# Performance work log

Hardware: AMD Instinct MI355X
Metric: run time of the kernel (lower is better)

## Reference

```python
import jax, jax.numpy as jnp
import numpy as np
import math

B, N, XD, ED, H = 8, 128, 256, 128, 8
DF = XD // H
FFX, FFE = 1024, 512


def _lin(x, w, b):
    return x @ w + b


def _ln(x, g, b):
    m = x.mean(-1, keepdims=True)
    v = ((x - m) ** 2).mean(-1, keepdims=True)
    return (x - m) / jnp.sqrt(v + 1e-5) * g + b


def setup_inputs() -> dict:
    key = jax.random.key(0)
    ks = jax.random.split(key, 16)
    d = {}
    d['x'] = jax.random.normal(ks[0], (B, N, XD), jnp.float32)
    d['e'] = jax.random.normal(ks[1], (B, N, N, ED), jnp.float32)
    wspecs = [('wq', (XD, XD)), ('wk', (XD, XD)), ('wv', (XD, XD)),
              ('wem', (ED, XD)), ('wea', (ED, XD)), ('wxo', (XD, XD)),
              ('weo', (XD, ED)), ('wx1', (XD, FFX)), ('wx2', (FFX, XD)),
              ('we1', (ED, FFE)), ('we2', (FFE, ED))]
    for i, (name, shp) in enumerate(wspecs):
        d[name] = jax.random.normal(ks[2 + i % 14], shp, jnp.float32) * 0.02
        d[name] = jax.random.normal(jax.random.fold_in(key, i + 10), shp, jnp.float32) * 0.02
    for name, dim in [('bq', XD), ('bk', XD), ('bv', XD), ('bem', XD), ('bea', XD),
                      ('bxo', XD), ('beo', ED), ('bx1', FFX), ('bx2', XD),
                      ('be1', FFE), ('be2', ED)]:
        d[name] = jnp.zeros((dim,), jnp.float32)
    d['gnx'] = jnp.ones((XD,), jnp.float32)
    d['bnx'] = jnp.zeros((XD,), jnp.float32)
    d['gne'] = jnp.ones((ED,), jnp.float32)
    d['bne'] = jnp.zeros((ED,), jnp.float32)
    return d


def reference(x, e, wq, wk, wv, wem, wea, wxo, weo, wx1, wx2, we1, we2,
              bq, bk, bv, bem, bea, bxo, beo, bx1, bx2, be1, be2,
              gnx, bnx, gne, bne):
    # --- NodeEdgeBlock ---
    Q = _lin(x, wq, bq).reshape(B, N, H, DF)
    K = _lin(x, wk, bk).reshape(B, N, H, DF)
    # per-channel outer product: (B, N_i, N_j, H, DF)
    Y = Q[:, :, None] * K[:, None] / math.sqrt(DF)
    E1 = _lin(e, wem, bem).reshape(B, N, N, H, DF)
    E2 = _lin(e, wea, bea).reshape(B, N, N, H, DF)
    Y = Y * (E1 + 1.0) + E2
    newE = _lin(Y.reshape(B, N, N, XD), weo, beo)
    attn = jax.nn.softmax(Y, axis=1)  # softmax over source-node axis i
    V = _lin(x, wv, bv := bv if False else bv).reshape(B, N, H, DF) if False else _lin(x, wv, bv).reshape(B, N, H, DF)
    wV = (attn * V[:, None]).sum(axis=1).reshape(B, N, XD)
    newX = _lin(wV, wxo, bxo)

    # --- FF blocks (dropout=0 => identity); note the SAME norm (norm2) is applied twice,
    # and the second residual uses the pre-norm input, matching the torch code. ---
    def ff(inp, new, w1, b1, w2, b2, g, bn):
        h = _ln(inp + new, g, bn)
        h = jax.nn.relu(_lin(h, w1, b1))
        h = _lin(h, w2, b2)
        return _ln(inp + h, g, bn)

    x_out = ff(x, newX, wx1, bx1, wx2, bx2, gnx, bnx)
    e_out = ff(e, newE, we1, be1, we2, be2, gne, bne)
    return (x_out, e_out)
```

## Files before the change

kernel.cpp:

```cpp
#include <hip/hip_runtime.h>


#define RSQRT_DF 0.17677669529663687f

typedef __attribute__((ext_vector_type(8))) short short8;
typedef __attribute__((ext_vector_type(4))) short short4v;
typedef __attribute__((ext_vector_type(4))) float f32x4;

__device__ __forceinline__ short f2bs(float f) {
    unsigned u = __float_as_uint(f);
    unsigned r = u + 0x7FFFu + ((u >> 16) & 1u);
    return (short)(r >> 16);
}
__device__ __forceinline__ float bs2f(short s) {
    return __uint_as_float(((unsigned)(unsigned short)s) << 16);
}

struct PackArgs {
    const float* W[11];
    short* Wp[11];
    int kdiv[11];
    int N[11];
    int start[12];
};

__global__ __launch_bounds__(256) void pack_all(PackArgs pa) {
    int g = blockIdx.x * 256 + threadIdx.x;
    if (g >= pa.start[11]) return;
    int i = 0;
    while (g >= pa.start[i + 1]) ++i;
    int local = g - pa.start[i];
    int kdiv = pa.kdiv[i], N = pa.N[i];
    int lane = local & 63, rest = local >> 6;
    int kb = rest % kdiv, nt = rest / kdiv;
    int n = nt * 16 + (lane & 15);
    int k0 = kb * 32 + ((lane >> 4) << 3);
    const float* W = pa.W[i];
    short8 v;
#pragma unroll
    for (int j = 0; j < 8; ++j) v[j] = f2bs(W[(size_t)(k0 + j) * N + n]);
    *(short8*)(pa.Wp[i] + (size_t)local * 8) = v;
}

__global__ __launch_bounds__(256) void qk_gemm(
    const float* __restrict__ x,
    const short* __restrict__ wqP, const short* __restrict__ wkP,
    const float* __restrict__ bq, const float* __restrict__ bk,
    float* __restrict__ Qb, float* __restrict__ Kb) {
    __shared__ short sXb[16 * 264];
    const int t = threadIdx.x, wave = t >> 6, lane = t & 63;
    const int quad = lane >> 4, l15 = lane & 15;
    const int m0 = (blockIdx.x & 63) * 16;
    const int isK = blockIdx.x >> 6;
    const short* wP = isK ? wkP : wqP;
    const float* bp = isK ? bk : bq;
    float* outp = isK ? Kb : Qb;

    const float4* x4 = (const float4*)(x + (size_t)m0 * 256);
    for (int g = t; g < 1024; g += 256) {
        float4 v = x4[g];
        int row = g >> 6, col4 = (g & 63) * 4;
        short4v sv = {f2bs(v.x), f2bs(v.y), f2bs(v.z), f2bs(v.w)};
        *(short4v*)(sXb + row * 264 + col4) = sv;
    }
    __syncthreads();

#pragma unroll 2
    for (int p = 0; p < 4; ++p) {
        int nt = wave * 4 + p;
        f32x4 acc = (f32x4){0.f, 0.f, 0.f, 0.f};
        const short* aB = sXb + l15 * 264 + quad * 8;
        const short* bB = wP + ((size_t)(nt * 8) * 64 + lane) * 8;
#pragma unroll
        for (int kb = 0; kb < 8; ++kb) {
            short8 a = *(const short8*)(aB + kb * 32);
            short8 w = *(const short8*)(bB + (size_t)kb * 512);
            acc = __builtin_amdgcn_mfma_f32_16x16x32_bf16(a, w, acc, 0, 0, 0);
        }
        int col = nt * 16 + l15;
        float bvv = bp[col];
#pragma unroll
        for (int r = 0; r < 4; ++r)
            outp[(size_t)(m0 + quad * 4 + r) * 256 + col] = acc[r] + bvv;
    }
}

__global__ __launch_bounds__(256, 3) void fused_main(
    const float* __restrict__ x, const float* __restrict__ e,
    const float* __restrict__ Qb, const float* __restrict__ Kb,
    const short* __restrict__ wvP, const short* __restrict__ wxoP,
    const short* __restrict__ wx1P, const short* __restrict__ wx2P,
    const short* __restrict__ wemP, const short* __restrict__ weaP,
    const short* __restrict__ weoP, const short* __restrict__ we1P,
    const short* __restrict__ we2P,
    const float* __restrict__ bv, const float* __restrict__ bxo,
    const float* __restrict__ bx1, const float* __restrict__ bx2,
    const float* __restrict__ bem, const float* __restrict__ bea,
    const float* __restrict__ beo, const float* __restrict__ be1,
    const float* __restrict__ be2,
    const float* __restrict__ gnx, const float* __restrict__ bnx,
    const float* __restrict__ gne, const float* __restrict__ bne,
    float* __restrict__ xout, float* __restrict__ eout) {
    __shared__ __align__(16) char ldsbuf[51200];
    const int t = threadIdx.x, wave = t >> 6, lane = t & 63;
    const int quad = lane >> 4, l15 = lane & 15;

    if (blockIdx.x < 64) {
        short* sXb = (short*)ldsbuf;
        short* sVb = (short*)(ldsbuf + 8448);
        short* sTbx = (short*)(ldsbuf + 16896);
        float* sRx = (float*)(ldsbuf + 25344);
        short* sH1x = (short*)(ldsbuf + 25344);
        float* sH2x = (float*)(ldsbuf + 25344);
        const int m0 = blockIdx.x * 16;

        const float4* x4 = (const float4*)(x + (size_t)m0 * 256);
        for (int g = t; g < 1024; g += 256) {
            float4 v = x4[g];
            int row = g >> 6, col4 = (g & 63) * 4;
            short4v sv = {f2bs(v.x), f2bs(v.y), f2bs(v.z), f2bs(v.w)};
            *(short4v*)(sXb + row * 264 + col4) = sv;
        }
        __syncthreads();

#pragma unroll 2
        for (int p = 0; p < 4; ++p) {
            int nt = wave * 4 + p;
            f32x4 acc = (f32x4){0.f, 0.f, 0.f, 0.f};
            const short* aB = sXb + l15 * 264 + quad * 8;
            const short* bB = wvP + ((size_t)(nt * 8) * 64 + lane) * 8;
#pragma unroll
            for (int kb = 0; kb < 8; ++kb) {
                short8 a = *(const short8*)(aB + kb * 32);
                short8 w = *(const short8*)(bB + (size_t)kb * 512);
                acc = __builtin_amdgcn_mfma_f32_16x16x32_bf16(a, w, acc, 0, 0, 0);
            }
            int col = nt * 16 + l15;
            float bvv = bv[col];
#pragma unroll
            for (int r = 0; r < 4; ++r)
                sVb[(quad * 4 + r) * 264 + col] = f2bs(acc[r] + bvv);
        }
        __syncthreads();

#pragma unroll 2
        for (int p = 0; p < 4; ++p) {
            int nt = wave * 4 + p;
            f32x4 acc = (f32x4){0.f, 0.f, 0.f, 0.f};
            const short* aB = sVb + l15 * 264 + quad * 8;
            const short* bB = wxoP + ((size_t)(nt * 8) * 64 + lane) * 8;
#pragma unroll
            for (int kb = 0; kb < 8; ++kb) {
                short8 a = *(const short8*)(aB + kb * 32);
                short8 w = *(const short8*)(bB + (size_t)kb * 512);
                acc = __builtin_amdgcn_mfma_f32_16x16x32_bf16(a, w, acc, 0, 0, 0);
            }
            int col = nt * 16 + l15;
            float bvv = bxo[col];
#pragma unroll
            for (int r = 0; r < 4; ++r)
                sRx[(quad * 4 + r) * 260 + col] = acc[r] + bvv;
        }
        __syncthreads();

        for (int rr = 0; rr < 4; ++rr) {
            int row = wave * 4 + rr;
            float v[4];
            float s1 = 0.f, s2 = 0.f;
#pragma unroll
            for (int k = 0; k < 4; ++k) {
                v[k] = bs2f(sXb[row * 264 + lane + 64 * k]) + sRx[row * 260 + lane + 64 * k];
                s1 += v[k]; s2 += v[k] * v[k];
            }
            for (int off = 32; off; off >>= 1) {
                s1 += __shfl_down(s1, off);
                s2 += __shfl_down(s2, off);
            }
            s1 = __shfl(s1, 0); s2 = __shfl(s2, 0);
            float mean = s1 * (1.f / 256.f);
            float var = s2 * (1.f / 256.f) - mean * mean;
            float rstd = rsqrtf(var + 1e-5f);
#pragma unroll
            for (int k = 0; k < 4; ++k)
                sTbx[row * 264 + lane + 64 * k] =
                    f2bs((v[k] - mean) * rstd * gnx[lane + 64 * k] + bnx[lane + 64 * k]);
        }
        __syncthreads();

        f32x4 accE[4];
#pragma unroll
        for (int p = 0; p < 4; ++p) accE[p] = (f32x4){0.f, 0.f, 0.f, 0.f};
        for (int half = 0; half < 2; ++half) {
#pragma unroll 2
            for (int p = 0; p < 8; ++p) {
                int ntg = half * 32 + wave * 8 + p;
                int coll = (wave * 8 + p) * 16 + l15;
                f32x4 acc = (f32x4){0.f, 0.f, 0.f, 0.f};
                const short* aB = sTbx + l15 * 264 + quad * 8;
                const short* bB = wx1P + ((size_t)(ntg * 8) * 64 + lane) * 8;
#pragma unroll
                for (int kb = 0; kb < 8; ++kb) {
                    short8 a = *(const short8*)(aB + kb * 32);
                    short8 w = *(const short8*)(bB + (size_t)kb * 512);
                    acc = __builtin_amdgcn_mfma_f32_16x16x32_bf16(a, w, acc, 0, 0, 0);
                }
                float bvv = bx1[ntg * 16 + l15];
#pragma unroll
                for (int r = 0; r < 4; ++r)
                    sH1x[(quad * 4 + r) * 520 + coll] = f2bs(fmaxf(acc[r] + bvv, 0.f));
            }
            __syncthreads();
#pragma unroll 2
            for (int p = 0; p < 4; ++p) {
                int nt = wave * 4 + p;
                const short* aB = sH1x + l15 * 520 + quad * 8;
                const short* bB = wx2P + ((size_t)(nt * 32 + half * 16) * 64 + lane) * 8;
#pragma unroll
                for (int kb = 0; kb < 16; ++kb) {
                    short8 a = *(const short8*)(aB + kb * 32);
                    short8 w = *(const short8*)(bB + (size_t)kb * 512);
                    accE[p] = __builtin_amdgcn_mfma_f32_16x16x32_bf16(a, w, accE[p], 0, 0, 0);
                }
            }
            __syncthreads();
        }
#pragma unroll
        for (int p = 0; p < 4; ++p) {
            int nt = wave * 4 + p;
            int col = nt * 16 + l15;
            float bvv = bx2[col];
#pragma unroll
            for (int r = 0; r < 4; ++r)
                sH2x[(quad * 4 + r) * 260 + col] = accE[p][r] + bvv;
        }
        __syncthreads();

        for (int rr = 0; rr < 4; ++rr) {
            int row = wave * 4 + rr;
            float v[4];
            float s1 = 0.f, s2 = 0.f;
#pragma unroll
            for (int k = 0; k < 4; ++k) {
                v[k] = bs2f(sXb[row * 264 + lane + 64 * k]) + sH2x[row * 260 + lane + 64 * k];
                s1 += v[k]; s2 += v[k] * v[k];
            }
            for (int off = 32; off; off >>= 1) {
                s1 += __shfl_down(s1, off);
                s2 += __shfl_down(s2, off);
            }
            s1 = __shfl(s1, 0); s2 = __shfl(s2, 0);
            float mean = s1 * (1.f / 256.f);
            float var = s2 * (1.f / 256.f) - mean * mean;
            float rstd = rsqrtf(var + 1e-5f);
#pragma unroll
            for (int k = 0; k < 4; ++k)
                xout[(size_t)(m0 + row) * 256 + lane + 64 * k] =
                    (v[k] - mean) * rstd * gnx[lane + 64 * k] + bnx[lane + 64 * k];
        }
        return;
    }

    short* sEb = (short*)ldsbuf;
    short* sTb = (short*)(ldsbuf + 8704);
    float* sR  = (float*)(ldsbuf + 17408);
    short* sH1 = (short*)(ldsbuf + 17408);
    short* sYb = (short*)(ldsbuf + 34304);
    float* sH2 = (float*)(ldsbuf + 34304);

    const int r0 = (blockIdx.x - 64) * 32;
    const int b = r0 >> 14;
    const int j0 = r0 & 127;

    float g0 = gne[lane], g1 = gne[lane + 64];
    float bn0 = bne[lane], bn1 = bne[lane + 64];

    float qk[2][4][4];
#pragma unroll
    for (int ntl = 0; ntl < 4; ++ntl) {
        const int col = (wave * 4 + ntl) * 16 + l15;
        const float q = Qb[(size_t)(r0 >> 7) * 256 + col] * RSQRT_DF;
#pragma unroll
        for (int mt = 0; mt < 2; ++mt) {
            const float* kp = Kb + (size_t)((b << 7) + j0 + mt * 16 + quad * 4) * 256 + col;
#pragma unroll
            for (int r = 0; r < 4; ++r) qk[mt][ntl][r] = q * kp[(size_t)r * 256];
        }
    }

    {
        const float4* e4 = (const float4*)(e + (size_t)r0 * 128);
        for (int g = t; g < 1024; g += 256) {
            float4 v = e4[g];
            int row = g >> 5, col4 = (g & 31) * 4;
            short4v sv = {f2bs(v.x), f2bs(v.y), f2bs(v.z), f2bs(v.w)};
            *(short4v*)(sEb + row * 136 + col4) = sv;
        }
    }
    __syncthreads();

    {
        short8 aE[2][4];
#pragma unroll
        for (int mt = 0; mt < 2; ++mt)
#pragma unroll
            for (int kb = 0; kb < 4; ++kb)
                aE[mt][kb] = *(const short8*)(sEb + (mt * 16 + l15) * 136 + quad * 8 + kb * 32);
#pragma unroll
        for (int ntl = 0; ntl < 4; ++ntl) {
            const int nt = wave * 4 + ntl;
            const short* b1 = wemP + ((size_t)(nt * 4) * 64 + lane) * 8;
            const short* b2 = weaP + ((size_t)(nt * 4) * 64 + lane) * 8;
            short8 w1[4], w2[4];
#pragma unroll
            for (int kb = 0; kb < 4; ++kb) {
                w1[kb] = *(const short8*)(b1 + (size_t)kb * 512);
                w2[kb] = *(const short8*)(b2 + (size_t)kb * 512);
            }
            const int col = nt * 16 + l15;
            const float bm = bem[col], ba = bea[col];
#pragma unroll
            for (int mt = 0; mt < 2; ++mt) {
                f32x4 a1 = (f32x4){0.f, 0.f, 0.f, 0.f};
                f32x4 a2 = (f32x4){0.f, 0.f, 0.f, 0.f};
#pragma unroll
                for (int kb = 0; kb < 4; ++kb) {
                    a1 = __builtin_amdgcn_mfma_f32_16x16x32_bf16(aE[mt][kb], w1[kb], a1, 0, 0, 0);
                    a2 = __builtin_amdgcn_mfma_f32_16x16x32_bf16(aE[mt][kb], w2[kb], a2, 0, 0, 0);
                }
#pragma unroll
                for (int r = 0; r < 4; ++r) {
                    int row = mt * 16 + quad * 4 + r;
                    float y = qk[mt][ntl][r] * (a1[r] + bm + 1.0f) + (a2[r] + ba);
                    sYb[row * 264 + col] = f2bs(y);
                }
            }
        }
    }
    __syncthreads();

    {
        short8 aY[2][8];
#pragma unroll
        for (int mt = 0; mt < 2; ++mt)
#pragma unroll
            for (int kb = 0; kb < 8; ++kb)
                aY[mt][kb] = *(const short8*)(sYb + (mt * 16 + l15) * 264 + quad * 8 + kb * 32);
#pragma unroll
        for (int ntl = 0; ntl < 2; ++ntl) {
            const int nt = wave * 2 + ntl;
            const short* bB = weoP + ((size_t)(nt * 8) * 64 + lane) * 8;
            short8 w[8];
#pragma unroll
            for (int kb = 0; kb < 8; ++kb) w[kb] = *(const short8*)(bB + (size_t)kb * 512);
            const int col = nt * 16 + l15;
            const float bo = beo[col];
#pragma unroll
            for (int mt = 0; mt < 2; ++mt) {
                f32x4 acc = (f32x4){0.f, 0.f, 0.f, 0.f};
#pragma unroll
                for (int kb = 0; kb < 8; ++kb)
                    acc = __builtin_amdgcn_mfma_f32_16x16x32_bf16(aY[mt][kb], w[kb], acc, 0, 0, 0);
#pragma unroll
                for (int r = 0; r < 4; ++r)
                    sR[(mt * 16 + quad * 4 + r) * 132 + col] = acc[r] + bo;
            }
        }
    }
    __syncthreads();

    for (int rr = 0; rr < 8; ++rr) {
        int row = wave * 8 + rr;
        float v0 = bs2f(sEb[row * 136 + lane]) + sR[row * 132 + lane];
        float v1 = bs2f(sEb[row * 136 + lane + 64]) + sR[row * 132 + lane + 64];
        float s1 = v0 + v1, s2 = v0 * v0 + v1 * v1;
        for (int off = 32; off; off >>= 1) {
            s1 += __shfl_down(s1, off);
            s2 += __shfl_down(s2, off);
        }
        s1 = __shfl(s1, 0); s2 = __shfl(s2, 0);
        float mean = s1 * 0.0078125f;
        float var = s2 * 0.0078125f - mean * mean;
        float rstd = rsqrtf(var + 1e-5f);
        sTb[row * 136 + lane]      = f2bs((v0 - mean) * rstd * g0 + bn0);
        sTb[row * 136 + lane + 64] = f2bs((v1 - mean) * rstd * g1 + bn1);
    }
    __syncthreads();

    f32x4 accE[4];
#pragma unroll
    for (int p = 0; p < 4; ++p) accE[p] = (f32x4){0.f, 0.f, 0.f, 0.f};

    for (int half = 0; half < 2; ++half) {
        short8 aT[2][4];
#pragma unroll
        for (int mt = 0; mt < 2; ++mt)
#pragma unroll
            for (int kb = 0; kb < 4; ++kb)
                aT[mt][kb] = *(const short8*)(sTb + (mt * 16 + l15) * 136 + quad * 8 + kb * 32);
#pragma unroll
        for (int ntl = 0; ntl < 4; ++ntl) {
            const int ntg = half * 16 + wave * 4 + ntl;
            const short* bB = we1P + ((size_t)(ntg * 4) * 64 + lane) * 8;
            short8 w[4];
#pragma unroll
            for (int kb = 0; kb < 4; ++kb) w[kb] = *(const short8*)(bB + (size_t)kb * 512);
            const int coll = (wave * 4 + ntl) * 16 + l15;
            const float bvv = be1[ntg * 16 + l15];
#pragma unroll
            for (int mt = 0; mt < 2; ++mt) {
                f32x4 acc = (f32x4){0.f, 0.f, 0.f, 0.f};
#pragma unroll
                for (int kb = 0; kb < 4; ++kb)
                    acc = __builtin_amdgcn_mfma_f32_16x16x32_bf16(aT[mt][kb], w[kb], acc, 0, 0, 0);
#pragma unroll
                for (int r = 0; r < 4; ++r)
                    sH1[(mt * 16 + quad * 4 + r) * 264 + coll] = f2bs(fmaxf(acc[r] + bvv, 0.f));
            }
        }
        __syncthreads();
        {
            short8 aH[2][8];
#pragma unroll
            for (int mt = 0; mt < 2; ++mt)
#pragma unroll
                for (int kb = 0; kb < 8; ++kb)
                    aH[mt][kb] = *(const short8*)(sH1 + (mt * 16 + l15) * 264 + quad * 8 + kb * 32);
#pragma unroll
            for (int ntl = 0; ntl < 2; ++ntl) {
                const int nt = wave * 2 + ntl;
                const short* bB = we2P + ((size_t)(nt * 16 + half * 8) * 64 + lane) * 8;
                short8 w[8];
#pragma unroll
                for (int kb = 0; kb < 8; ++kb) w[kb] = *(const short8*)(bB + (size_t)kb * 512);
#pragma unroll
                for (int mt = 0; mt < 2; ++mt) {
#pragma unroll
                    for (int kb = 0; kb < 8; ++kb)
                        accE[ntl * 2 + mt] = __builtin_amdgcn_mfma_f32_16x16x32_bf16(
                            aH[mt][kb], w[kb], accE[ntl * 2 + mt], 0, 0, 0);
                }
            }
        }
        __syncthreads();
    }
#pragma unroll
    for (int ntl = 0; ntl < 2; ++ntl)
#pragma unroll
        for (int mt = 0; mt < 2; ++mt) {
            const int nt = wave * 2 + ntl;
            const int col = nt * 16 + l15;
            const float bvv = be2[col];
#pragma unroll
            for (int r = 0; r < 4; ++r)
                sH2[(mt * 16 + quad * 4 + r) * 132 + col] = accE[ntl * 2 + mt][r] + bvv;
        }
    __syncthreads();

    for (int rr = 0; rr < 8; ++rr) {
        int row = wave * 8 + rr;
        float v0 = bs2f(sEb[row * 136 + lane]) + sH2[row * 132 + lane];
        float v1 = bs2f(sEb[row * 136 + lane + 64]) + sH2[row * 132 + lane + 64];
        float s1 = v0 + v1, s2 = v0 * v0 + v1 * v1;
        for (int off = 32; off; off >>= 1) {
            s1 += __shfl_down(s1, off);
            s2 += __shfl_down(s2, off);
        }
        s1 = __shfl(s1, 0); s2 = __shfl(s2, 0);
        float mean = s1 * 0.0078125f;
        float var = s2 * 0.0078125f - mean * mean;
        float rstd = rsqrtf(var + 1e-5f);
        size_t o = (size_t)(r0 + row) * 128;
        eout[o + lane]      = (v0 - mean) * rstd * g0 + bn0;
        eout[o + lane + 64] = (v1 - mean) * rstd * g1 + bn1;
    }
}

extern "C" void kernel_launch(void* const* d_in, const int* in_sizes, int n_in,
                              void* d_out, int out_size, void* d_ws, size_t ws_size,
                              hipStream_t stream) {
    const float* x   = (const float*)d_in[0];
    const float* e   = (const float*)d_in[1];
    const float* wq  = (const float*)d_in[2];
    const float* wk  = (const float*)d_in[3];
    const float* wv  = (const float*)d_in[4];
    const float* wem = (const float*)d_in[5];
    const float* wea = (const float*)d_in[6];
    const float* wxo = (const float*)d_in[7];
    const float* weo = (const float*)d_in[8];
    const float* wx1 = (const float*)d_in[9];
    const float* wx2 = (const float*)d_in[10];
    const float* we1 = (const float*)d_in[11];
    const float* we2 = (const float*)d_in[12];
    const float* bq  = (const float*)d_in[13];
    const float* bk  = (const float*)d_in[14];
    const float* bv  = (const float*)d_in[15];
    const float* bem = (const float*)d_in[16];
    const float* bea = (const float*)d_in[17];
    const float* bxo = (const float*)d_in[18];
    const float* beo = (const float*)d_in[19];
    const float* bx1 = (const float*)d_in[20];
    const float* bx2 = (const float*)d_in[21];
    const float* be1 = (const float*)d_in[22];
    const float* be2 = (const float*)d_in[23];
    const float* gnx = (const float*)d_in[24];
    const float* bnx = (const float*)d_in[25];
    const float* gne = (const float*)d_in[26];
    const float* bne = (const float*)d_in[27];

    float* out = (float*)d_out;

    float* ws = (float*)d_ws;
    float* Qb = ws;
    float* Kb = Qb + 262144;
    short* base = (short*)(Kb + 262144);
    short* wqP  = base;
    short* wkP  = wqP + 65536;
    short* wvP  = wkP + 65536;
    short* wxoP = wvP + 65536;
    short* wx1P = wxoP + 65536;
    short* wx2P = wx1P + 262144;
    short* wemP = wx2P + 262144;
    short* weaP = wemP + 32768;
    short* weoP = weaP + 32768;
    short* we1P = weoP + 32768;
    short* we2P = we1P + 65536;

    PackArgs pa;
    const float* Ws[11] = {wq, wk, wv, wxo, wx1, wx2, wem, wea, weo, we1, we2};
    short* Wps[11] = {wqP, wkP, wvP, wxoP, wx1P, wx2P, wemP, weaP, weoP, we1P, we2P};
    int Ks[11] = {256, 256, 256, 256, 256, 1024, 128, 128, 256, 128, 512};
    int Ns[11] = {256, 256, 256, 256, 1024, 256, 256, 256, 128, 512, 128};
    int acc = 0;
    for (int i = 0; i < 11; ++i) {
        pa.W[i] = Ws[i];
        pa.Wp[i] = Wps[i];
        pa.kdiv[i] = Ks[i] >> 5;
        pa.N[i] = Ns[i];
        pa.start[i] = acc;
        acc += (Ns[i] >> 4) * (Ks[i] >> 5) * 64;
    }
    pa.start[11] = acc;
    pack_all<<<(acc + 255) / 256, 256, 0, stream>>>(pa);

    qk_gemm<<<128, 256, 0, stream>>>(x, wqP, wkP, bq, bk, Qb, Kb);

    fused_main<<<4160, 256, 0, stream>>>(
        x, e, Qb, Kb, wvP, wxoP, wx1P, wx2P, wemP, weaP, weoP, we1P, we2P,
        bv, bxo, bx1, bx2, bem, bea, beo, be1, be2,
        gnx, bnx, gne, bne, out, out + 262144);
}
```

Measured before the change: 299.6 us.

## Shrink LDS footprint to raise occupancy to four blocks per CU

Cuts the fused kernel's shared-memory buffer from 51200 to 34304 bytes and raises launch bounds from 3 to 4 blocks per CU. To fit, the FFN hidden layers are split into four quarter chunks instead of two halves, and intermediate residual and FFN outputs are kept in LDS as bf16 instead of fp32. A-operand fragments are hoisted into registers once per GEMM, and the weight loads are batched. The intent is more waves in flight to hide latency. In exchange there are more barriers per FFN, extra bf16 rounding of the pre-LayerNorm residuals, and register pressure that could spill under the tighter launch bound.

```diff
diff --git a/kernel.cpp b/kernel.cpp
--- a/kernel.cpp
+++ b/kernel.cpp
@@ -85,7 +85,7 @@
     }
 }
 
-__global__ __launch_bounds__(256, 3) void fused_main(
+__global__ __launch_bounds__(256, 4) void fused_main(
     const float* __restrict__ x, const float* __restrict__ e,
     const float* __restrict__ Qb, const float* __restrict__ Kb,
     const short* __restrict__ wvP, const short* __restrict__ wxoP,
@@ -101,17 +101,17 @@
     const float* __restrict__ gnx, const float* __restrict__ bnx,
     const float* __restrict__ gne, const float* __restrict__ bne,
     float* __restrict__ xout, float* __restrict__ eout) {
-    __shared__ __align__(16) char ldsbuf[51200];
+    __shared__ __align__(16) char ldsbuf[34304];
     const int t = threadIdx.x, wave = t >> 6, lane = t & 63;
     const int quad = lane >> 4, l15 = lane & 15;
 
     if (blockIdx.x < 64) {
-        short* sXb = (short*)ldsbuf;
-        short* sVb = (short*)(ldsbuf + 8448);
+        short* sXb  = (short*)ldsbuf;
+        short* sVb  = (short*)(ldsbuf + 8448);
         short* sTbx = (short*)(ldsbuf + 16896);
-        float* sRx = (float*)(ldsbuf + 25344);
+        short* sRx  = (short*)(ldsbuf + 25344);
         short* sH1x = (short*)(ldsbuf + 25344);
-        float* sH2x = (float*)(ldsbuf + 25344);
+        short* sH2x = (short*)(ldsbuf + 25344);
         const int m0 = blockIdx.x * 16;
 
         const float4* x4 = (const float4*)(x + (size_t)m0 * 256);
@@ -123,43 +123,53 @@
         }
         __syncthreads();
 
-#pragma unroll 2
-        for (int p = 0; p < 4; ++p) {
-            int nt = wave * 4 + p;
-            f32x4 acc = (f32x4){0.f, 0.f, 0.f, 0.f};
-            const short* aB = sXb + l15 * 264 + quad * 8;
-            const short* bB = wvP + ((size_t)(nt * 8) * 64 + lane) * 8;
-#pragma unroll
-            for (int kb = 0; kb < 8; ++kb) {
-                short8 a = *(const short8*)(aB + kb * 32);
-                short8 w = *(const short8*)(bB + (size_t)kb * 512);
-                acc = __builtin_amdgcn_mfma_f32_16x16x32_bf16(a, w, acc, 0, 0, 0);
-            }
-            int col = nt * 16 + l15;
-            float bvv = bv[col];
-#pragma unroll
-            for (int r = 0; r < 4; ++r)
-                sVb[(quad * 4 + r) * 264 + col] = f2bs(acc[r] + bvv);
-        }
-        __syncthreads();
-
-#pragma unroll 2
-        for (int p = 0; p < 4; ++p) {
-            int nt = wave * 4 + p;
-            f32x4 acc = (f32x4){0.f, 0.f, 0.f, 0.f};
-            const short* aB = sVb + l15 * 264 + quad * 8;
-            const short* bB = wxoP + ((size_t)(nt * 8) * 64 + lane) * 8;
-#pragma unroll
-            for (int kb = 0; kb < 8; ++kb) {
-                short8 a = *(const short8*)(aB + kb * 32);
-                short8 w = *(const short8*)(bB + (size_t)kb * 512);
-                acc = __builtin_amdgcn_mfma_f32_16x16x32_bf16(a, w, acc, 0, 0, 0);
-            }
-            int col = nt * 16 + l15;
-            float bvv = bxo[col];
-#pragma unroll
-            for (int r = 0; r < 4; ++r)
-                sRx[(quad * 4 + r) * 260 + col] = acc[r] + bvv;
+        {
+            short8 aX[8];
+#pragma unroll
+            for (int kb = 0; kb < 8; ++kb)
+                aX[kb] = *(const short8*)(sXb + l15 * 264 + quad * 8 + kb * 32);
+#pragma unroll
+            for (int ntl = 0; ntl < 4; ++ntl) {
+                int nt = wave * 4 + ntl;
+                const short* bB = wvP + ((size_t)(nt * 8) * 64 + lane) * 8;
+                short8 w[8];
+#pragma unroll
+                for (int kb = 0; kb < 8; ++kb) w[kb] = *(const short8*)(bB + (size_t)kb * 512);
+                f32x4 acc = (f32x4){0.f, 0.f, 0.f, 0.f};
+#pragma unroll
+                for (int kb = 0; kb < 8; ++kb)
+                    acc = __builtin_amdgcn_mfma_f32_16x16x32_bf16(aX[kb], w[kb], acc, 0, 0, 0);
+                int col = nt * 16 + l15;
+                float bvv = bv[col];
+#pragma unroll
+                for (int r = 0; r < 4; ++r)
+                    sVb[(quad * 4 + r) * 264 + col] = f2bs(acc[r] + bvv);
+            }
+        }
+        __syncthreads();
+
+        {
+            short8 aV[8];
+#pragma unroll
+            for (int kb = 0; kb < 8; ++kb)
+                aV[kb] = *(const short8*)(sVb + l15 * 264 + quad * 8 + kb * 32);
+#pragma unroll
+            for (int ntl = 0; ntl < 4; ++ntl) {
+                int nt = wave * 4 + ntl;
+                const short* bB = wxoP + ((size_t)(nt * 8) * 64 + lane) * 8;
+                short8 w[8];
+#pragma unroll
+                for (int kb = 0; kb < 8; ++kb) w[kb] = *(const short8*)(bB + (size_t)kb * 512);
+                f32x4 acc = (f32x4){0.f, 0.f, 0.f, 0.f};
+#pragma unroll
+                for (int kb = 0; kb < 8; ++kb)
+                    acc = __builtin_amdgcn_mfma_f32_16x16x32_bf16(aV[kb], w[kb], acc, 0, 0, 0);
+                int col = nt * 16 + l15;
+                float bvv = bxo[col];
+#pragma unroll
+                for (int r = 0; r < 4; ++r)
+                    sRx[(quad * 4 + r) * 264 + col] = f2bs(acc[r] + bvv);
+            }
         }
         __syncthreads();
 
@@ -169,7 +179,7 @@
             float s1 = 0.f, s2 = 0.f;
 #pragma unroll
             for (int k = 0; k < 4; ++k) {
-                v[k] = bs2f(sXb[row * 264 + lane + 64 * k]) + sRx[row * 260 + lane + 64 * k];
+                v[k] = bs2f(sXb[row * 264 + lane + 64 * k]) + bs2f(sRx[row * 264 + lane + 64 * k]);
                 s1 += v[k]; s2 += v[k] * v[k];
             }
             for (int off = 32; off; off >>= 1) {
@@ -187,51 +197,59 @@
         }
         __syncthreads();
 
+        short8 aTx[8];
+#pragma unroll
+        for (int kb = 0; kb < 8; ++kb)
+            aTx[kb] = *(const short8*)(sTbx + l15 * 264 + quad * 8 + kb * 32);
         f32x4 accE[4];
 #pragma unroll
         for (int p = 0; p < 4; ++p) accE[p] = (f32x4){0.f, 0.f, 0.f, 0.f};
-        for (int half = 0; half < 2; ++half) {
-#pragma unroll 2
-            for (int p = 0; p < 8; ++p) {
-                int ntg = half * 32 + wave * 8 + p;
-                int coll = (wave * 8 + p) * 16 + l15;
+
+        for (int q = 0; q < 4; ++q) {
+#pragma unroll
+            for (int ntl = 0; ntl < 4; ++ntl) {
+                int ntg = q * 16 + wave * 4 + ntl;
+                const short* bB = wx1P + ((size_t)(ntg * 8) * 64 + lane) * 8;
+                short8 w[8];
+#pragma unroll
+                for (int kb = 0; kb < 8; ++kb) w[kb] = *(const short8*)(bB + (size_t)kb * 512);
                 f32x4 acc = (f32x4){0.f, 0.f, 0.f, 0.f};
-                const short* aB = sTbx + l15 * 264 + quad * 8;
-                const short* bB = wx1P + ((size_t)(ntg * 8) * 64 + lane) * 8;
-#pragma unroll
-                for (int kb = 0; kb < 8; ++kb) {
-                    short8 a = *(const short8*)(aB + kb * 32);
-                    short8 w = *(const short8*)(bB + (size_t)kb * 512);
-                    acc = __builtin_amdgcn_mfma_f32_16x16x32_bf16(a, w, acc, 0, 0, 0);
+#pragma unroll
+                for (int kb = 0; kb < 8; ++kb)
+                    acc = __builtin_amdgcn_mfma_f32_16x16x32_bf16(aTx[kb], w[kb], acc, 0, 0, 0);
+                int coll = (wave * 4 + ntl) * 16 + l15;
+                float bvv = bx1[ntg * 16 + l15];
+#pragma unroll
+                for (int r = 0; r < 4; ++r)
+                    sH1x[(quad * 4 + r) * 264 + coll] = f2bs(fmaxf(acc[r] + bvv, 0.f));
+            }
+            __syncthreads();
+            {
+                short8 aHx[8];
+#pragma unroll
+                for (int kb = 0; kb < 8; ++kb)
+                    aHx[kb] = *(const short8*)(sH1x + l15 * 264 + quad * 8 + kb * 32);
+#pragma unroll
+                for (int ntl = 0; ntl < 4; ++ntl) {
+                    int nt = wave * 4 + ntl;
+                    const short* bB = wx2P + ((size_t)(nt * 32 + q * 8) * 64 + lane) * 8;
+                    short8 w[8];
+#pragma unroll
+                    for (int kb = 0; kb < 8; ++kb) w[kb] = *(const short8*)(bB + (size_t)kb * 512);
+#pragma unroll
+                    for (int kb = 0; kb < 8; ++kb)
+                        accE[ntl] = __builtin_amdgcn_mfma_f32_16x16x32_bf16(aHx[kb], w[kb], accE[ntl], 0, 0, 0);
                 }
-                float bvv = bx1[ntg * 16 + l15];
-#pragma unroll
-                for (int r = 0; r < 4; ++r)
-                    sH1x[(quad * 4 + r) * 520 + coll] = f2bs(fmaxf(acc[r] + bvv, 0.f));
             }
             __syncthreads();
-#pragma unroll 2
-            for (int p = 0; p < 4; ++p) {
-                int nt = wave * 4 + p;
-                const short* aB = sH1x + l15 * 520 + quad * 8;
-                const short* bB = wx2P + ((size_t)(nt * 32 + half * 16) * 64 + lane) * 8;
-#pragma unroll
-                for (int kb = 0; kb < 16; ++kb) {
-                    short8 a = *(const short8*)(aB + kb * 32);
-                    short8 w = *(const short8*)(bB + (size_t)kb * 512);
-                    accE[p] = __builtin_amdgcn_mfma_f32_16x16x32_bf16(a, w, accE[p], 0, 0, 0);
-                }
-            }
-            __syncthreads();
-        }
-#pragma unroll
-        for (int p = 0; p < 4; ++p) {
-            int nt = wave * 4 + p;
-            int col = nt * 16 + l15;
+        }
+#pragma unroll
+        for (int ntl = 0; ntl < 4; ++ntl) {
+            int col = (wave * 4 + ntl) * 16 + l15;
             float bvv = bx2[col];
 #pragma unroll
             for (int r = 0; r < 4; ++r)
-                sH2x[(quad * 4 + r) * 260 + col] = accE[p][r] + bvv;
+                sH2x[(quad * 4 + r) * 264 + col] = f2bs(accE[ntl][r] + bvv);
         }
         __syncthreads();
 
@@ -241,7 +259,7 @@
             float s1 = 0.f, s2 = 0.f;
 #pragma unroll
             for (int k = 0; k < 4; ++k) {
-                v[k] = bs2f(sXb[row * 264 + lane + 64 * k]) + sH2x[row * 260 + lane + 64 * k];
+                v[k] = bs2f(sXb[row * 264 + lane + 64 * k]) + bs2f(sH2x[row * 264 + lane + 64 * k]);
                 s1 += v[k]; s2 += v[k] * v[k];
             }
             for (int off = 32; off; off >>= 1) {
@@ -261,11 +279,11 @@
     }
 
     short* sEb = (short*)ldsbuf;
+    short* sYb = (short*)(ldsbuf + 8704);
     short* sTb = (short*)(ldsbuf + 8704);
-    float* sR  = (float*)(ldsbuf + 17408);
-    short* sH1 = (short*)(ldsbuf + 17408);
-    short* sYb = (short*)(ldsbuf + 34304);
-    float* sH2 = (float*)(ldsbuf + 34304);
+    float* sH2 = (float*)(ldsbuf + 8704);
+    short* sR  = (short*)(ldsbuf + 25600);
+    short* sH1 = (short*)(ldsbuf + 25600);
 
     const int r0 = (blockIdx.x - 64) * 32;
     const int b = r0 >> 14;
@@ -362,7 +380,7 @@
                     acc = __builtin_amdgcn_mfma_f32_16x16x32_bf16(aY[mt][kb], w[kb], acc, 0, 0, 0);
 #pragma unroll
                 for (int r = 0; r < 4; ++r)
-                    sR[(mt * 16 + quad * 4 + r) * 132 + col] = acc[r] + bo;
+                    sR[(mt * 16 + quad * 4 + r) * 136 + col] = f2bs(acc[r] + bo);
             }
         }
     }
@@ -370,8 +388,8 @@
 
     for (int rr = 0; rr < 8; ++rr) {
         int row = wave * 8 + rr;
-        float v0 = bs2f(sEb[row * 136 + lane]) + sR[row * 132 + lane];
-        float v1 = bs2f(sEb[row * 136 + lane + 64]) + sR[row * 132 + lane + 64];
+        float v0 = bs2f(sEb[row * 136 + lane]) + bs2f(sR[row * 136 + lane]);
+        float v1 = bs2f(sEb[row * 136 + lane + 64]) + bs2f(sR[row * 136 + lane + 64]);
         float s1 = v0 + v1, s2 = v0 * v0 + v1 * v1;
         for (int off = 32; off; off >>= 1) {
             s1 += __shfl_down(s1, off);
@@ -386,25 +404,25 @@
     }
     __syncthreads();
 
+    short8 aT[2][4];
+#pragma unroll
+    for (int mt = 0; mt < 2; ++mt)
+#pragma unroll
+        for (int kb = 0; kb < 4; ++kb)
+            aT[mt][kb] = *(const short8*)(sTb + (mt * 16 + l15) * 136 + quad * 8 + kb * 32);
     f32x4 accE[4];
 #pragma unroll
     for (int p = 0; p < 4; ++p) accE[p] = (f32x4){0.f, 0.f, 0.f, 0.f};
 
-    for (int half = 0; half < 2; ++half) {
-        short8 aT[2][4];
-#pragma unroll
-        for (int mt = 0; mt < 2; ++mt)
-#pragma unroll
-            for (int kb = 0; kb < 4; ++kb)
-                aT[mt][kb] = *(const short8*)(sTb + (mt * 16 + l15) * 136 + quad * 8 + kb * 32);
-#pragma unroll
-        for (int ntl = 0; ntl < 4; ++ntl) {
-            const int ntg = half * 16 + wave * 4 + ntl;
+    for (int q = 0; q < 4; ++q) {
+#pragma unroll
+        for (int ntl = 0; ntl < 2; ++ntl) {
+            const int ntg = q * 8 + wave * 2 + ntl;
             const short* bB = we1P + ((size_t)(ntg * 4) * 64 + lane) * 8;
             short8 w[4];
 #pragma unroll
             for (int kb = 0; kb < 4; ++kb) w[kb] = *(const short8*)(bB + (size_t)kb * 512);
-            const int coll = (wave * 4 + ntl) * 16 + l15;
+            const int coll = (wave * 2 + ntl) * 16 + l15;
             const float bvv = be1[ntg * 16 + l15];
 #pragma unroll
             for (int mt = 0; mt < 2; ++mt) {
@@ -414,28 +432,28 @@
                     acc = __builtin_amdgcn_mfma_f32_16x16x32_bf16(aT[mt][kb], w[kb], acc, 0, 0, 0);
 #pragma unroll
                 for (int r = 0; r < 4; ++r)
-                    sH1[(mt * 16 + quad * 4 + r) * 264 + coll] = f2bs(fmaxf(acc[r] + bvv, 0.f));
+                    sH1[(mt * 16 + quad * 4 + r) * 136 + coll] = f2bs(fmaxf(acc[r] + bvv, 0.f));
             }
         }
         __syncthreads();
         {
-            short8 aH[2][8];
+            short8 aH[2][4];
 #pragma unroll
             for (int mt = 0; mt < 2; ++mt)
 #pragma unroll
-                for (int kb = 0; kb < 8; ++kb)
-                    aH[mt][kb] = *(const short8*)(sH1 + (mt * 16 + l15) * 264 + quad * 8 + kb * 32);
+                for (int kb = 0; kb < 4; ++kb)
+                    aH[mt][kb] = *(const short8*)(sH1 + (mt * 16 + l15) * 136 + quad * 8 + kb * 32);
 #pragma unroll
             for (int ntl = 0; ntl < 2; ++ntl) {
                 const int nt = wave * 2 + ntl;
-                const short* bB = we2P + ((size_t)(nt * 16 + half * 8) * 64 + lane) * 8;
-                short8 w[8];
-#pragma unroll
-                for (int kb = 0; kb < 8; ++kb) w[kb] = *(const short8*)(bB + (size_t)kb * 512);
+                const short* bB = we2P + ((size_t)(nt * 16 + q * 4) * 64 + lane) * 8;
+                short8 w[4];
+#pragma unroll
+                for (int kb = 0; kb < 4; ++kb) w[kb] = *(const short8*)(bB + (size_t)kb * 512);
 #pragma unroll
                 for (int mt = 0; mt < 2; ++mt) {
 #pragma unroll
-                    for (int kb = 0; kb < 8; ++kb)
+                    for (int kb = 0; kb < 4; ++kb)
                         accE[ntl * 2 + mt] = __builtin_amdgcn_mfma_f32_16x16x32_bf16(
                             aH[mt][kb], w[kb], accE[ntl * 2 + mt], 0, 0, 0);
                 }
@@ -447,8 +465,7 @@
     for (int ntl = 0; ntl < 2; ++ntl)
 #pragma unroll
         for (int mt = 0; mt < 2; ++mt) {
-            const int nt = wave * 2 + ntl;
-            const int col = nt * 16 + l15;
+            const int col = (wave * 2 + ntl) * 16 + l15;
             const float bvv = be2[col];
 #pragma unroll
             for (int r = 0; r < 4; ++r)
```

Result: slower. 355.4 us (+18.6%).
